# Optimization experiments

Hardware: AMD Instinct MI355X
Metric: run time of the kernel (lower is better)

## Reference

```python
import jax, jax.numpy as jnp
import numpy as np

N_NODES = 50000
N_EDGES = 800000
N_GRAPHS = 128
F_IN = 256
H = 256
DH = 64
NC = 2


def _lin_init(k, fin, fout):
    s = 1.0 / np.sqrt(fin)
    return jax.random.uniform(k, (fin, fout), jnp.float32, -s, s)


def setup_inputs() -> dict:
    key = jax.random.key(0)
    ks = jax.random.split(key, 12)
    x = jax.random.normal(ks[0], (N_NODES, F_IN), jnp.float32)
    edge_index = jax.random.randint(ks[1], (2, N_EDGES), 0, N_NODES, jnp.int32)
    edge_attr = jax.random.uniform(ks[2], (N_EDGES,), jnp.float32)
    batch = jnp.sort(jax.random.randint(ks[3], (N_NODES,), 0, N_GRAPHS, jnp.int32))
    return {
        "x": x, "edge_index": edge_index, "edge_attr": edge_attr, "batch": batch,
        "W1": _lin_init(ks[4], F_IN, H), "b1": jnp.zeros((H,), jnp.float32),
        "W2": _lin_init(ks[5], H, H), "b2": jnp.zeros((H,), jnp.float32),
        "W3": _lin_init(ks[6], H, H), "b3": jnp.zeros((H,), jnp.float32),
        "L1w": _lin_init(ks[7], H, DH), "L1b": jnp.zeros((DH,), jnp.float32),
        "L2w": _lin_init(ks[8], DH, DH // 2), "L2b": jnp.zeros((DH // 2,), jnp.float32),
        "L3w": _lin_init(ks[9], DH // 2, NC), "L3b": jnp.zeros((NC,), jnp.float32),
    }


def reference(x, edge_index, edge_attr, batch, W1, b1, W2, b2, W3, b3,
              L1w, L1b, L2w, L2b, L3w, L3b):
    src, dst = edge_index[0], edge_index[1]
    # GCN normalization with self loops (weight 1): deg includes self-loop
    deg = jax.ops.segment_sum(edge_attr, dst, num_segments=N_NODES) + 1.0
    dinv = jnp.where(deg > 0, jax.lax.rsqrt(deg), 0.0)
    norm = dinv[src] * edge_attr * dinv[dst]          # [E]
    self_coef = dinv * dinv                            # [N], self-loop norm

    def gcn(h, W, b):
        h = h @ W                                      # [N, H]
        agg = jax.ops.segment_sum(norm[:, None] * h[src], dst, num_segments=N_NODES)
        return agg + self_coef[:, None] * h + b

    c1 = gcn(x, W1, b1)
    h = jax.nn.relu(c1)                                # dropout is eval-mode no-op
    c2 = gcn(h, W2, b2)
    h = jax.nn.relu(c2)
    c3 = gcn(h, W3, b3)
    h = jax.nn.relu(c3)

    # global mean pool over graphs
    sums = jax.ops.segment_sum(h, batch, num_segments=N_GRAPHS)
    cnt = jax.ops.segment_sum(jnp.ones((N_NODES,), h.dtype), batch, num_segments=N_GRAPHS)
    pooled = sums / jnp.clip(cnt, 1.0)[:, None]        # [B, H]

    o = jax.nn.relu(pooled @ L1w + L1b)
    o = jax.nn.relu(o @ L2w + L2b)
    out = jax.nn.relu(o @ L3w + L3b)                   # [B, NC]
    return (out, pooled, c1, c2, c3)
```

## Files before the change

kernel.cpp:

```cpp
#include <hip/hip_runtime.h>

#define N_NODES  50000
#define N_EDGES  800000
#define N_GRAPHS 128
#define FDIM     256

typedef __attribute__((ext_vector_type(8))) short short8;
typedef __attribute__((ext_vector_type(4))) float f32x4;

__device__ __forceinline__ unsigned short f2bf(float f) {
    union { float f; unsigned int u; } v; v.f = f;
    unsigned int x = v.u;
    unsigned int r = (x + 0x7FFFu + ((x >> 16) & 1u)) >> 16;
    return (unsigned short)r;
}

__device__ __forceinline__ float bf2f(unsigned short u) {
    union { unsigned int i; float f; } v;
    v.i = ((unsigned int)u) << 16;
    return v.f;
}


__global__ void k_zero(float* deg, int* cnt, int n) {
    int i = blockIdx.x * blockDim.x + threadIdx.x;
    if (i < n) { deg[i] = 0.0f; cnt[i] = 0; }
}

__global__ void k_deg(const int* __restrict__ dst, const float* __restrict__ ea,
                      float* deg, int* cnt, int E) {
    int e = blockIdx.x * blockDim.x + threadIdx.x;
    if (e < E) {
        int d = dst[e];
        atomicAdd(&deg[d], ea[e]);
        atomicAdd(&cnt[d], 1);
    }
}

__global__ void k_dinv(const float* __restrict__ deg, float* dinv, int n) {
    int i = blockIdx.x * blockDim.x + threadIdx.x;
    if (i < n) dinv[i] = rsqrtf(deg[i] + 1.0f);
}


__global__ __launch_bounds__(1024) void k_scan1(const int* __restrict__ cnt,
                                                int* row_ptr, int* partial, int n) {
    __shared__ int buf[2][1024];
    int tid = threadIdx.x;
    int i = blockIdx.x * 1024 + tid;
    int v = (i < n) ? cnt[i] : 0;
    buf[0][tid] = v;
    __syncthreads();
    int pb = 0;
    for (int off = 1; off < 1024; off <<= 1) {
        int t = buf[pb][tid];
        if (tid >= off) t += buf[pb][tid - off];
        buf[1 - pb][tid] = t;
        pb = 1 - pb;
        __syncthreads();
    }
    int incl = buf[pb][tid];
    if (i < n) row_ptr[i] = incl - v;
    if (tid == 1023) partial[blockIdx.x] = incl;
}

__global__ void k_scan2(int* partial, int nb, int* totalp) {
    int l = threadIdx.x;
    int v = (l < nb) ? partial[l] : 0;
    int orig = v;
    for (int off = 1; off < 64; off <<= 1) {
        int t = __shfl_up(v, off);
        if (l >= off) v += t;
    }
    if (l < nb) partial[l] = v - orig;
    if (l == nb - 1) *totalp = v;
}

__global__ void k_scan3(int* row_ptr, int* cursor, const int* __restrict__ partial, int n) {
    int i = blockIdx.x * blockDim.x + threadIdx.x;
    if (i < n) {
        int v = row_ptr[i] + partial[i >> 10];
        row_ptr[i] = v;
        cursor[i] = v;
    }
}


__global__ void k_scatter(const int* __restrict__ src, const int* __restrict__ dst,
                          const float* __restrict__ ea,
                          const float* __restrict__ dinv,
                          int* cursor, int2* cv, int E) {
    int e = blockIdx.x * blockDim.x + threadIdx.x;
    if (e < E) {
        int d = dst[e];
        int s = src[e];
        int p = atomicAdd(&cursor[d], 1);
        cv[p] = make_int2(s, __float_as_int(ea[e] * dinv[s]));
    }
}

__global__ void k_repack(const float* __restrict__ W, unsigned short* __restrict__ Wp) {
    int t = blockIdx.x * blockDim.x + threadIdx.x;
    int j = t & 7;
    int l = (t >> 3) & 63;
    int c = (t >> 9) & 15;
    int s = t >> 13;
    int k = s * 32 + ((l >> 4) * 8) + j;
    int n = c * 16 + (l & 15);
    Wp[t] = f2bf(W[k * 256 + n]);
}

__global__ void k_xcast(const float* __restrict__ x, unsigned short* __restrict__ Xb, int n4) {
    int i = blockIdx.x * blockDim.x + threadIdx.x;
    if (i < n4) {
        float4 v = ((const float4*)x)[i];
        ((ushort4*)Xb)[i] = make_ushort4(f2bf(v.x), f2bf(v.y), f2bf(v.z), f2bf(v.w));
    }
}

__global__ __launch_bounds__(256) void k_agg_bf(const unsigned short* __restrict__ Hb,
                                                const int* __restrict__ rowptr,
                                                const int2* __restrict__ cv,
                                                const float* __restrict__ dinv,
                                                unsigned short* __restrict__ S, int M) {
    int wave = threadIdx.x >> 6;
    int lane = threadIdx.x & 63;
    int n = blockIdx.x * 4 + wave;
    if (n >= M) return;
    int c4 = lane * 4;

    float a0 = 0.f, a1 = 0.f, a2 = 0.f, a3 = 0.f;
    int e0 = rowptr[n], e1 = rowptr[n + 1];
    int e = e0;
#pragma unroll 1
    for (; e + 4 <= e1; e += 4) {
        int2 p0 = cv[e], p1 = cv[e + 1], p2 = cv[e + 2], p3 = cv[e + 3];
        ushort4 h0 = *(const ushort4*)(Hb + (size_t)p0.x * 256 + c4);
        ushort4 h1 = *(const ushort4*)(Hb + (size_t)p1.x * 256 + c4);
        ushort4 h2 = *(const ushort4*)(Hb + (size_t)p2.x * 256 + c4);
        ushort4 h3 = *(const ushort4*)(Hb + (size_t)p3.x * 256 + c4);
        float v0 = __int_as_float(p0.y), v1 = __int_as_float(p1.y);
        float v2 = __int_as_float(p2.y), v3 = __int_as_float(p3.y);
        a0 = fmaf(v0, bf2f(h0.x), a0); a1 = fmaf(v0, bf2f(h0.y), a1);
        a2 = fmaf(v0, bf2f(h0.z), a2); a3 = fmaf(v0, bf2f(h0.w), a3);
        a0 = fmaf(v1, bf2f(h1.x), a0); a1 = fmaf(v1, bf2f(h1.y), a1);
        a2 = fmaf(v1, bf2f(h1.z), a2); a3 = fmaf(v1, bf2f(h1.w), a3);
        a0 = fmaf(v2, bf2f(h2.x), a0); a1 = fmaf(v2, bf2f(h2.y), a1);
        a2 = fmaf(v2, bf2f(h2.z), a2); a3 = fmaf(v2, bf2f(h2.w), a3);
        a0 = fmaf(v3, bf2f(h3.x), a0); a1 = fmaf(v3, bf2f(h3.y), a1);
        a2 = fmaf(v3, bf2f(h3.z), a2); a3 = fmaf(v3, bf2f(h3.w), a3);
    }
#pragma unroll 1
    for (; e < e1; e++) {
        int2 p = cv[e];
        float v = __int_as_float(p.y);
        ushort4 h = *(const ushort4*)(Hb + (size_t)p.x * 256 + c4);
        a0 = fmaf(v, bf2f(h.x), a0); a1 = fmaf(v, bf2f(h.y), a1);
        a2 = fmaf(v, bf2f(h.z), a2); a3 = fmaf(v, bf2f(h.w), a3);
    }
    float di = dinv[n];
    float sc = di * di;
    ushort4 hn = *(const ushort4*)(Hb + (size_t)n * 256 + c4);
    *(ushort4*)(S + (size_t)n * 256 + c4) =
        make_ushort4(f2bf(fmaf(di, a0, sc * bf2f(hn.x))), f2bf(fmaf(di, a1, sc * bf2f(hn.y))),
                     f2bf(fmaf(di, a2, sc * bf2f(hn.z))), f2bf(fmaf(di, a3, sc * bf2f(hn.w))));
}

template<bool RELU>
__global__ __launch_bounds__(256) void k_agg(const float* __restrict__ H,
                                             const int* __restrict__ rowptr,
                                             const int2* __restrict__ cv,
                                             const float* __restrict__ dinv,
                                             unsigned short* __restrict__ S, int M) {
    int wave = threadIdx.x >> 6;
    int lane = threadIdx.x & 63;
    int n = blockIdx.x * 4 + wave;
    if (n >= M) return;
    int f4 = lane * 4;

    float a0 = 0.f, a1 = 0.f, a2 = 0.f, a3 = 0.f;
    int e0 = rowptr[n], e1 = rowptr[n + 1];
    for (int e = e0; e < e1; e++) {
        int2 p = cv[e];
        float v = __int_as_float(p.y);
        float4 h = *(const float4*)(H + (size_t)p.x * 256 + f4);
        if (RELU) {
            h.x = fmaxf(h.x, 0.f); h.y = fmaxf(h.y, 0.f);
            h.z = fmaxf(h.z, 0.f); h.w = fmaxf(h.w, 0.f);
        }
        a0 = fmaf(v, h.x, a0); a1 = fmaf(v, h.y, a1);
        a2 = fmaf(v, h.z, a2); a3 = fmaf(v, h.w, a3);
    }
    float di = dinv[n];
    float sc = di * di;
    float4 hn = *(const float4*)(H + (size_t)n * 256 + f4);
    if (RELU) {
        hn.x = fmaxf(hn.x, 0.f); hn.y = fmaxf(hn.y, 0.f);
        hn.z = fmaxf(hn.z, 0.f); hn.w = fmaxf(hn.w, 0.f);
    }
    *(ushort4*)(S + (size_t)n * 256 + f4) =
        make_ushort4(f2bf(fmaf(di, a0, sc * hn.x)), f2bf(fmaf(di, a1, sc * hn.y)),
                     f2bf(fmaf(di, a2, sc * hn.z)), f2bf(fmaf(di, a3, sc * hn.w)));
}

__global__ __launch_bounds__(256, 2) void k_gemm2(const unsigned short* __restrict__ S,
                                                  const unsigned short* __restrict__ Wp,
                                                  const float* __restrict__ bias,
                                                  float* __restrict__ C,
                                                  unsigned short* __restrict__ Hb,
                                                  int nTiles) {
    int wave = threadIdx.x >> 6;
    int lane = threadIdx.x & 63;
    int q    = lane >> 4;
    int m16  = lane & 15;
    const short8* wp8 = (const short8*)Wp;

    short8 b[8][4];
#pragma unroll
    for (int s = 0; s < 8; s++)
#pragma unroll
        for (int cc = 0; cc < 4; cc++)
            b[s][cc] = wp8[(s * 16 + wave * 4 + cc) * 64 + lane];

    float bv[4];
#pragma unroll
    for (int cc = 0; cc < 4; cc++) bv[cc] = bias[(wave * 4 + cc) * 16 + m16];

#pragma unroll 1
    for (int rt = blockIdx.x; rt < nTiles; rt += gridDim.x) {
        int arow = rt * 16 + m16;
        short8 a[8];
#pragma unroll
        for (int s = 0; s < 8; s++)
            a[s] = *(const short8*)(S + (size_t)arow * 256 + s * 32 + q * 8);

        f32x4 acc[4];
#pragma unroll
        for (int cc = 0; cc < 4; cc++) acc[cc] = (f32x4){0.f, 0.f, 0.f, 0.f};

#pragma unroll
        for (int s = 0; s < 8; s++)
#pragma unroll
            for (int cc = 0; cc < 4; cc++)
                acc[cc] = __builtin_amdgcn_mfma_f32_16x16x32_bf16(a[s], b[s][cc], acc[cc], 0, 0, 0);

        int orow0 = rt * 16 + q * 4;
#pragma unroll
        for (int cc = 0; cc < 4; cc++) {
            int colv = (wave * 4 + cc) * 16 + m16;
#pragma unroll
            for (int r = 0; r < 4; r++)
                C[(size_t)(orow0 + r) * 256 + colv] = acc[cc][r] + bv[cc];
        }
        if (Hb != nullptr) {
#pragma unroll
            for (int cc = 0; cc < 4; cc++) {
                int colv = (wave * 4 + cc) * 16 + m16;
#pragma unroll
                for (int r = 0; r < 4; r++)
                    Hb[(size_t)(orow0 + r) * 256 + colv] = f2bf(fmaxf(acc[cc][r] + bv[cc], 0.f));
            }
        }
    }
}

__global__ __launch_bounds__(1024) void k_pool(const float* __restrict__ C3,
                                               const int* __restrict__ batch, int N,
                                               float* __restrict__ pooled) {
    int g = blockIdx.x;
    __shared__ int range[2];
    __shared__ float part[4][256];
    if (threadIdx.x == 0 && threadIdx.y == 0) {
        int lo = 0, hi = N;
        while (lo < hi) { int mid = (lo + hi) >> 1; if (batch[mid] < g) lo = mid + 1; else hi = mid; }
        range[0] = lo;
        int lo2 = lo, hi2 = N;
        while (lo2 < hi2) { int mid = (lo2 + hi2) >> 1; if (batch[mid] < g + 1) lo2 = mid + 1; else hi2 = mid; }
        range[1] = lo2;
    }
    __syncthreads();
    int start = range[0], end = range[1];
    int f = threadIdx.x;
    float s = 0.f;
    for (int i = start + threadIdx.y; i < end; i += 4)
        s += fmaxf(C3[(size_t)i * 256 + f], 0.f);
    part[threadIdx.y][f] = s;
    __syncthreads();
    if (threadIdx.y == 0) {
        float tot = part[0][f] + part[1][f] + part[2][f] + part[3][f];
        int cnt = end - start;
        pooled[g * 256 + f] = tot / (float)(cnt > 0 ? cnt : 1);
    }
}

__global__ __launch_bounds__(64) void k_mlp(const float* __restrict__ pooled,
                                            const float* __restrict__ L1w,
                                            const float* __restrict__ L1b,
                                            const float* __restrict__ L2w,
                                            const float* __restrict__ L2b,
                                            const float* __restrict__ L3w,
                                            const float* __restrict__ L3b,
                                            float* __restrict__ out) {
    int g = blockIdx.x;
    int j = threadIdx.x;
    __shared__ float o1[64];
    __shared__ float o2[32];
    float s = L1b[j];
    const float* p = pooled + g * 256;
    for (int k = 0; k < 256; k++) s = fmaf(p[k], L1w[k * 64 + j], s);
    o1[j] = fmaxf(s, 0.f);
    __syncthreads();
    if (j < 32) {
        float s2 = L2b[j];
        for (int k = 0; k < 64; k++) s2 = fmaf(o1[k], L2w[k * 32 + j], s2);
        o2[j] = fmaxf(s2, 0.f);
    }
    __syncthreads();
    if (j < 2) {
        float s3 = L3b[j];
        for (int k = 0; k < 32; k++) s3 = fmaf(o2[k], L3w[k * 2 + j], s3);
        out[g * 2 + j] = fmaxf(s3, 0.f);
    }
}

extern "C" void kernel_launch(void* const* d_in, const int* in_sizes, int n_in,
                              void* d_out, int out_size, void* d_ws, size_t ws_size,
                              hipStream_t stream) {
    const float* x   = (const float*)d_in[0];
    const int*   ei  = (const int*)d_in[1];
    const float* ea  = (const float*)d_in[2];
    const int*   bat = (const int*)d_in[3];
    const float* W1  = (const float*)d_in[4];
    const float* b1  = (const float*)d_in[5];
    const float* W2  = (const float*)d_in[6];
    const float* b2  = (const float*)d_in[7];
    const float* W3  = (const float*)d_in[8];
    const float* b3  = (const float*)d_in[9];
    const float* L1w = (const float*)d_in[10];
    const float* L1b = (const float*)d_in[11];
    const float* L2w = (const float*)d_in[12];
    const float* L2b = (const float*)d_in[13];
    const float* L3w = (const float*)d_in[14];
    const float* L3b = (const float*)d_in[15];

    const int N = N_NODES, E = N_EDGES;
    const int* srcp = ei;
    const int* dstp = ei + E;

    float* out_p    = (float*)d_out;
    float* pooled_p = out_p + 256;
    float* c1_p     = out_p + 33024;
    float* c2_p     = c1_p + (size_t)N * FDIM;
    float* c3_p     = c2_p + (size_t)N * FDIM;

    char* ws = (char*)d_ws;
    size_t off = 0;
    unsigned short* Sb  = (unsigned short*)(ws + off); off += (size_t)(N + 64) * FDIM * 2;
    unsigned short* Wp1 = (unsigned short*)(ws + off); off += 65536 * 2;
    unsigned short* Wp2 = (unsigned short*)(ws + off); off += 65536 * 2;
    unsigned short* Wp3 = (unsigned short*)(ws + off); off += 65536 * 2;
    float* dinv    = (float*)(ws + off); off += (size_t)N * 4;
    float* deg     = (float*)(ws + off); off += (size_t)N * 4;
    int*   cnt     = (int*)(ws + off);   off += (size_t)N * 4;
    int*   row_ptr = (int*)(ws + off);   off += ((size_t)N + 16) * 4;
    int*   cursor  = (int*)(ws + off);   off += (size_t)N * 4;
    int2*  cv      = (int2*)(ws + off);  off += (size_t)E * 8;
    int*   partial = (int*)(ws + off);   off += 64 * 4;
    unsigned short* Hb = (unsigned short*)(ws + off); off += (size_t)(N + 64) * FDIM * 2;
    bool use_bf = (ws_size >= off);
    (void)n_in; (void)in_sizes; (void)out_size;

    int nb256 = (N + 255) / 256;
    int eb256 = (E + 255) / 256;
    int nb1024 = (N + 1023) / 1024;

    k_zero<<<nb256, 256, 0, stream>>>(deg, cnt, N);
    k_deg<<<eb256, 256, 0, stream>>>(dstp, ea, deg, cnt, E);
    k_dinv<<<nb256, 256, 0, stream>>>(deg, dinv, N);
    k_scan1<<<nb1024, 1024, 0, stream>>>(cnt, row_ptr, partial, N);
    k_scan2<<<1, 64, 0, stream>>>(partial, nb1024, row_ptr + N);
    k_scan3<<<nb256, 256, 0, stream>>>(row_ptr, cursor, partial, N);
    k_scatter<<<eb256, 256, 0, stream>>>(srcp, dstp, ea, dinv, cursor, cv, E);

    k_repack<<<256, 256, 0, stream>>>(W1, Wp1);
    k_repack<<<256, 256, 0, stream>>>(W2, Wp2);
    k_repack<<<256, 256, 0, stream>>>(W3, Wp3);

    int agg_blocks  = (N + 3) / 4;
    int nTiles      = (N + 15) / 16;
    int gemm_blocks = 512;

    if (use_bf) {
        k_xcast<<<(N * 64 + 255) / 256, 256, 0, stream>>>(x, Hb, N * 64);
        k_agg_bf<<<agg_blocks, 256, 0, stream>>>(Hb, row_ptr, cv, dinv, Sb, N);
        k_gemm2<<<gemm_blocks, 256, 0, stream>>>(Sb, Wp1, b1, c1_p, Hb, nTiles);
        k_agg_bf<<<agg_blocks, 256, 0, stream>>>(Hb, row_ptr, cv, dinv, Sb, N);
        k_gemm2<<<gemm_blocks, 256, 0, stream>>>(Sb, Wp2, b2, c2_p, Hb, nTiles);
        k_agg_bf<<<agg_blocks, 256, 0, stream>>>(Hb, row_ptr, cv, dinv, Sb, N);
        k_gemm2<<<gemm_blocks, 256, 0, stream>>>(Sb, Wp3, b3, c3_p, nullptr, nTiles);
    } else {
        k_agg<false><<<agg_blocks, 256, 0, stream>>>(x, row_ptr, cv, dinv, Sb, N);
        k_gemm2<<<gemm_blocks, 256, 0, stream>>>(Sb, Wp1, b1, c1_p, nullptr, nTiles);
        k_agg<true><<<agg_blocks, 256, 0, stream>>>(c1_p, row_ptr, cv, dinv, Sb, N);
        k_gemm2<<<gemm_blocks, 256, 0, stream>>>(Sb, Wp2, b2, c2_p, nullptr, nTiles);
        k_agg<true><<<agg_blocks, 256, 0, stream>>>(c2_p, row_ptr, cv, dinv, Sb, N);
        k_gemm2<<<gemm_blocks, 256, 0, stream>>>(Sb, Wp3, b3, c3_p, nullptr, nTiles);
    }

    dim3 pb(256, 4);
    k_pool<<<N_GRAPHS, pb, 0, stream>>>(c3_p, bat, N, pooled_p);
    k_mlp<<<N_GRAPHS, 64, 0, stream>>>(pooled_p, L1w, L1b, L2w, L2b, L3w, L3b, out_p);
}
```

Baseline: 634.8 us.

## Split bf16 aggregation into column passes with edge-parallel sub-waves; fuse small prep kernels

The bf16 SpMM aggregation now launches four column passes of 64 features each. Within a wave, four 16-lane subgroups handle interleaved edges and are combined with shuffle reductions. This narrows each gathered row segment to 128 bytes, puts more independent edge loads in flight per node and may improve cache locality per pass. The cost is that the CSR row pointers and edge list are read four times, plus extra shuffles. Separately, the dinv computation is folded into the first scan kernel and the three weight repacks are merged into one launch, which cuts launch count.

```diff
diff --git a/kernel.cpp b/kernel.cpp
--- a/kernel.cpp
+++ b/kernel.cpp
@@ -37,17 +37,15 @@
     }
 }
 
-__global__ void k_dinv(const float* __restrict__ deg, float* dinv, int n) {
-    int i = blockIdx.x * blockDim.x + threadIdx.x;
-    if (i < n) dinv[i] = rsqrtf(deg[i] + 1.0f);
-}
-
 
 __global__ __launch_bounds__(1024) void k_scan1(const int* __restrict__ cnt,
+                                                const float* __restrict__ deg,
+                                                float* __restrict__ dinv,
                                                 int* row_ptr, int* partial, int n) {
     __shared__ int buf[2][1024];
     int tid = threadIdx.x;
     int i = blockIdx.x * 1024 + tid;
+    if (i < n) dinv[i] = rsqrtf(deg[i] + 1.0f);
     int v = (i < n) ? cnt[i] : 0;
     buf[0][tid] = v;
     __syncthreads();
@@ -99,15 +97,19 @@
     }
 }
 
-__global__ void k_repack(const float* __restrict__ W, unsigned short* __restrict__ Wp) {
-    int t = blockIdx.x * blockDim.x + threadIdx.x;
+__global__ void k_repack3(const float* __restrict__ W1, const float* __restrict__ W2,
+                          const float* __restrict__ W3, unsigned short* __restrict__ Wp) {
+    int tid = blockIdx.x * blockDim.x + threadIdx.x;
+    int w = tid >> 16;
+    int t = tid & 65535;
+    const float* W = (w == 0) ? W1 : ((w == 1) ? W2 : W3);
     int j = t & 7;
     int l = (t >> 3) & 63;
     int c = (t >> 9) & 15;
     int s = t >> 13;
     int k = s * 32 + ((l >> 4) * 8) + j;
     int n = c * 16 + (l & 15);
-    Wp[t] = f2bf(W[k * 256 + n]);
+    Wp[tid] = f2bf(W[k * 256 + n]);
 }
 
 __global__ void k_xcast(const float* __restrict__ x, unsigned short* __restrict__ Xb, int n4) {
@@ -118,52 +120,60 @@
     }
 }
 
-__global__ __launch_bounds__(256) void k_agg_bf(const unsigned short* __restrict__ Hb,
+__global__ __launch_bounds__(256) void k_agg_cs(const unsigned short* __restrict__ Hb,
                                                 const int* __restrict__ rowptr,
                                                 const int2* __restrict__ cv,
                                                 const float* __restrict__ dinv,
-                                                unsigned short* __restrict__ S, int M) {
+                                                unsigned short* __restrict__ S,
+                                                int M, int rowBlocks) {
+    int pass = blockIdx.x / rowBlocks;
+    int rb   = blockIdx.x - pass * rowBlocks;
     int wave = threadIdx.x >> 6;
     int lane = threadIdx.x & 63;
-    int n = blockIdx.x * 4 + wave;
+    int sub  = lane >> 4;
+    int l16  = lane & 15;
+    int n = rb * 4 + wave;
     if (n >= M) return;
-    int c4 = lane * 4;
+    int cbase = pass * 64 + l16 * 4;
 
     float a0 = 0.f, a1 = 0.f, a2 = 0.f, a3 = 0.f;
     int e0 = rowptr[n], e1 = rowptr[n + 1];
-    int e = e0;
-#pragma unroll 1
-    for (; e + 4 <= e1; e += 4) {
-        int2 p0 = cv[e], p1 = cv[e + 1], p2 = cv[e + 2], p3 = cv[e + 3];
-        ushort4 h0 = *(const ushort4*)(Hb + (size_t)p0.x * 256 + c4);
-        ushort4 h1 = *(const ushort4*)(Hb + (size_t)p1.x * 256 + c4);
-        ushort4 h2 = *(const ushort4*)(Hb + (size_t)p2.x * 256 + c4);
-        ushort4 h3 = *(const ushort4*)(Hb + (size_t)p3.x * 256 + c4);
-        float v0 = __int_as_float(p0.y), v1 = __int_as_float(p1.y);
-        float v2 = __int_as_float(p2.y), v3 = __int_as_float(p3.y);
-        a0 = fmaf(v0, bf2f(h0.x), a0); a1 = fmaf(v0, bf2f(h0.y), a1);
-        a2 = fmaf(v0, bf2f(h0.z), a2); a3 = fmaf(v0, bf2f(h0.w), a3);
-        a0 = fmaf(v1, bf2f(h1.x), a0); a1 = fmaf(v1, bf2f(h1.y), a1);
-        a2 = fmaf(v1, bf2f(h1.z), a2); a3 = fmaf(v1, bf2f(h1.w), a3);
-        a0 = fmaf(v2, bf2f(h2.x), a0); a1 = fmaf(v2, bf2f(h2.y), a1);
-        a2 = fmaf(v2, bf2f(h2.z), a2); a3 = fmaf(v2, bf2f(h2.w), a3);
-        a0 = fmaf(v3, bf2f(h3.x), a0); a1 = fmaf(v3, bf2f(h3.y), a1);
-        a2 = fmaf(v3, bf2f(h3.z), a2); a3 = fmaf(v3, bf2f(h3.w), a3);
-    }
-#pragma unroll 1
-    for (; e < e1; e++) {
+
+    int e = e0 + sub;
+    for (; e + 4 < e1; e += 8) {
+        int2 pA = cv[e];
+        int2 pB = cv[e + 4];
+        ushort4 hA = *(const ushort4*)(Hb + (size_t)pA.x * 256 + cbase);
+        ushort4 hB = *(const ushort4*)(Hb + (size_t)pB.x * 256 + cbase);
+        float vA = __int_as_float(pA.y);
+        float vB = __int_as_float(pB.y);
+        a0 = fmaf(vA, bf2f(hA.x), a0); a1 = fmaf(vA, bf2f(hA.y), a1);
+        a2 = fmaf(vA, bf2f(hA.z), a2); a3 = fmaf(vA, bf2f(hA.w), a3);
+        a0 = fmaf(vB, bf2f(hB.x), a0); a1 = fmaf(vB, bf2f(hB.y), a1);
+        a2 = fmaf(vB, bf2f(hB.z), a2); a3 = fmaf(vB, bf2f(hB.w), a3);
+    }
+    if (e < e1) {
         int2 p = cv[e];
+        ushort4 h = *(const ushort4*)(Hb + (size_t)p.x * 256 + cbase);
         float v = __int_as_float(p.y);
-        ushort4 h = *(const ushort4*)(Hb + (size_t)p.x * 256 + c4);
         a0 = fmaf(v, bf2f(h.x), a0); a1 = fmaf(v, bf2f(h.y), a1);
         a2 = fmaf(v, bf2f(h.z), a2); a3 = fmaf(v, bf2f(h.w), a3);
     }
-    float di = dinv[n];
-    float sc = di * di;
-    ushort4 hn = *(const ushort4*)(Hb + (size_t)n * 256 + c4);
-    *(ushort4*)(S + (size_t)n * 256 + c4) =
-        make_ushort4(f2bf(fmaf(di, a0, sc * bf2f(hn.x))), f2bf(fmaf(di, a1, sc * bf2f(hn.y))),
-                     f2bf(fmaf(di, a2, sc * bf2f(hn.z))), f2bf(fmaf(di, a3, sc * bf2f(hn.w))));
+    a0 += __shfl_xor(a0, 16); a0 += __shfl_xor(a0, 32);
+    a1 += __shfl_xor(a1, 16); a1 += __shfl_xor(a1, 32);
+    a2 += __shfl_xor(a2, 16); a2 += __shfl_xor(a2, 32);
+    a3 += __shfl_xor(a3, 16); a3 += __shfl_xor(a3, 32);
+
+    if (sub == 0) {
+        float di = dinv[n];
+        float sc = di * di;
+        ushort4 hn = *(const ushort4*)(Hb + (size_t)n * 256 + cbase);
+        *(ushort4*)(S + (size_t)n * 256 + cbase) =
+            make_ushort4(f2bf(fmaf(di, a0, sc * bf2f(hn.x))),
+                         f2bf(fmaf(di, a1, sc * bf2f(hn.y))),
+                         f2bf(fmaf(di, a2, sc * bf2f(hn.z))),
+                         f2bf(fmaf(di, a3, sc * bf2f(hn.w))));
+    }
 }
 
 template<bool RELU>
@@ -376,29 +386,27 @@
 
     k_zero<<<nb256, 256, 0, stream>>>(deg, cnt, N);
     k_deg<<<eb256, 256, 0, stream>>>(dstp, ea, deg, cnt, E);
-    k_dinv<<<nb256, 256, 0, stream>>>(deg, dinv, N);
-    k_scan1<<<nb1024, 1024, 0, stream>>>(cnt, row_ptr, partial, N);
+    k_scan1<<<nb1024, 1024, 0, stream>>>(cnt, deg, dinv, row_ptr, partial, N);
     k_scan2<<<1, 64, 0, stream>>>(partial, nb1024, row_ptr + N);
     k_scan3<<<nb256, 256, 0, stream>>>(row_ptr, cursor, partial, N);
     k_scatter<<<eb256, 256, 0, stream>>>(srcp, dstp, ea, dinv, cursor, cv, E);
-
-    k_repack<<<256, 256, 0, stream>>>(W1, Wp1);
-    k_repack<<<256, 256, 0, stream>>>(W2, Wp2);
-    k_repack<<<256, 256, 0, stream>>>(W3, Wp3);
-
-    int agg_blocks  = (N + 3) / 4;
+    k_repack3<<<768, 256, 0, stream>>>(W1, W2, W3, Wp1);
+
+    int rowBlocks   = (N + 3) / 4;
+    int agg_grid    = rowBlocks * 4;
     int nTiles      = (N + 15) / 16;
     int gemm_blocks = 512;
 
     if (use_bf) {
         k_xcast<<<(N * 64 + 255) / 256, 256, 0, stream>>>(x, Hb, N * 64);
-        k_agg_bf<<<agg_blocks, 256, 0, stream>>>(Hb, row_ptr, cv, dinv, Sb, N);
+        k_agg_cs<<<agg_grid, 256, 0, stream>>>(Hb, row_ptr, cv, dinv, Sb, N, rowBlocks);
         k_gemm2<<<gemm_blocks, 256, 0, stream>>>(Sb, Wp1, b1, c1_p, Hb, nTiles);
-        k_agg_bf<<<agg_blocks, 256, 0, stream>>>(Hb, row_ptr, cv, dinv, Sb, N);
+        k_agg_cs<<<agg_grid, 256, 0, stream>>>(Hb, row_ptr, cv, dinv, Sb, N, rowBlocks);
         k_gemm2<<<gemm_blocks, 256, 0, stream>>>(Sb, Wp2, b2, c2_p, Hb, nTiles);
-        k_agg_bf<<<agg_blocks, 256, 0, stream>>>(Hb, row_ptr, cv, dinv, Sb, N);
+        k_agg_cs<<<agg_grid, 256, 0, stream>>>(Hb, row_ptr, cv, dinv, Sb, N, rowBlocks);
         k_gemm2<<<gemm_blocks, 256, 0, stream>>>(Sb, Wp3, b3, c3_p, nullptr, nTiles);
     } else {
+        int agg_blocks = (N + 3) / 4;
         k_agg<false><<<agg_blocks, 256, 0, stream>>>(x, row_ptr, cv, dinv, Sb, N);
         k_gemm2<<<gemm_blocks, 256, 0, stream>>>(Sb, Wp1, b1, c1_p, nullptr, nTiles);
         k_agg<true><<<agg_blocks, 256, 0, stream>>>(c1_p, row_ptr, cv, dinv, Sb, N);
```

Result: slower. 729.7 us (+14.9%).
